# Kernel tuning notes

Hardware: AMD Instinct MI355X
Metric: run time of the kernel (lower is better)

## Reference

```python
import jax, jax.numpy as jnp
import numpy as np

N0, N1, N2 = 65536, 8192, 1024   # node counts per depth (pool factor 8, as in original m1*2=8)
DEG = 6                          # avg degree of k-space neighbor graphs
K = 10                           # number of Gaussian kernels in GMMConv


def _pool_graph(n_fine):
    # bidirectional edges between each group of 8 nodes and its representative (last node of group)
    mem = jnp.arange(n_fine)
    rep = (mem // 8) * 8 + 7
    return jnp.concatenate([mem, rep]), jnp.concatenate([rep, mem])


def setup_inputs() -> dict:
    key = jax.random.key(0)
    ks = list(jax.random.split(key, 40))
    E1, E2, E3 = DEG * N0, DEG * N1, DEG * N2
    d = {}
    d['n_feat'] = jax.random.normal(ks[0], (N0, 2), jnp.float32)
    d['src1'] = jax.random.randint(ks[1], (E1,), 0, N0)
    d['dst1'] = jax.random.randint(ks[2], (E1,), 0, N0)
    d['pkor1'] = 0.5 * jax.random.normal(ks[3], (E1, 2), jnp.float32)
    d['src2'] = jax.random.randint(ks[4], (E2,), 0, N1)
    d['dst2'] = jax.random.randint(ks[5], (E2,), 0, N1)
    d['pkor2'] = 0.5 * jax.random.normal(ks[6], (E2, 2), jnp.float32)
    d['src3'] = jax.random.randint(ks[7], (E3,), 0, N2)
    d['dst3'] = jax.random.randint(ks[8], (E3,), 0, N2)
    d['pkor3'] = 0.5 * jax.random.normal(ks[9], (E3, 2), jnp.float32)
    d['pm1_src'], d['pm1_dst'] = _pool_graph(N0)
    d['pm2_src'], d['pm2_dst'] = _pool_graph(N1)
    d['idx1'] = jnp.arange(N1) * 8 + 7
    d['idx2'] = jnp.arange(N2) * 8 + 7

    def lin(k, fi, fo):
        return jax.random.normal(k, (fi, K * fo), jnp.float32) / np.float32(np.sqrt(fi * K))

    d['W1'] = lin(ks[10], 2, 32)
    d['mu1'] = jax.random.normal(ks[11], (K, 2), jnp.float32)
    d['is1'] = jax.random.uniform(ks[12], (K, 2), jnp.float32, 0.5, 1.5)
    d['b1'] = 0.01 * jax.random.normal(ks[13], (32,), jnp.float32)
    d['W2'] = lin(ks[14], 32, 64)
    d['mu2'] = jax.random.normal(ks[15], (K, 2), jnp.float32)
    d['is2'] = jax.random.uniform(ks[16], (K, 2), jnp.float32, 0.5, 1.5)
    d['W3'] = lin(ks[17], 64, 128)
    d['mu3'] = jax.random.normal(ks[18], (K, 2), jnp.float32)
    d['is3'] = jax.random.uniform(ks[19], (K, 2), jnp.float32, 0.5, 1.5)
    d['W4'] = lin(ks[20], 192, 64)
    d['mu4'] = jax.random.normal(ks[21], (K, 2), jnp.float32)
    d['is4'] = jax.random.uniform(ks[22], (K, 2), jnp.float32, 0.5, 1.5)
    d['W5'] = lin(ks[23], 96, 40)
    d['mu5'] = jax.random.normal(ks[24], (K, 2), jnp.float32)
    d['is5'] = jax.random.uniform(ks[25], (K, 2), jnp.float32, 0.5, 1.5)
    d['b5'] = 0.01 * jax.random.normal(ks[26], (40,), jnp.float32)
    return d


def gmm_conv(x, W, mu, inv_sigma, src, dst, pseudo, n, bias=None):
    # DGL GMMConv, aggregator 'mean': h=fc(x) -> (N,K,F); gaussian edge weights over 2D pseudo coords
    h = (x @ W).reshape(x.shape[0], K, -1)                                   # (N,K,F)
    diff = pseudo[:, None, :] - mu[None, :, :]                               # (E,K,2)
    gw = jnp.exp(-0.5 * jnp.sum(diff * diff * (inv_sigma[None] ** 2), -1))   # (E,K)
    msg = h[src] * gw[:, :, None]                                            # (E,K,F)
    s = jax.ops.segment_sum(msg, dst, num_segments=n)
    deg = jax.ops.segment_sum(jnp.ones(dst.shape, x.dtype), dst, num_segments=n)
    out = jnp.sum(s / jnp.maximum(deg, 1.0)[:, None, None], axis=1)          # mean over edges, sum over kernels
    return out if bias is None else out + bias


def max_reduce(h, src, dst, n):
    # DGL update_all(copy_u, max): nodes with no in-edges get 0
    m = jax.ops.segment_max(h[src], dst, num_segments=n)
    deg = jax.ops.segment_sum(jnp.ones(dst.shape, h.dtype), dst, num_segments=n)
    return jnp.where(deg[:, None] > 0, m, jnp.zeros((), h.dtype))


def reference(n_feat, src1, dst1, pkor1, src2, dst2, pkor2, src3, dst3, pkor3,
              pm1_src, pm1_dst, pm2_src, pm2_dst, idx1, idx2,
              W1, mu1, is1, b1, W2, mu2, is2, W3, mu3, is3,
              W4, mu4, is4, W5, mu5, is5, b5):
    # encoder
    out0 = jax.nn.relu(gmm_conv(n_feat, W1, mu1, is1, src1, dst1, pkor1, N0, b1))      # (N0,32) skip0
    h = max_reduce(out0, pm1_src, pm1_dst, N0)[idx1]                                    # MaxPool -> (N1,32)
    out1 = jax.nn.relu(gmm_conv(h, W2, mu2, is2, src2, dst2, pkor2, N1))                # (N1,64) skip1
    h = max_reduce(out1, pm2_src, pm2_dst, N1)[idx2]                                    # MaxPool -> (N2,64)
    out2 = jax.nn.relu(gmm_conv(h, W3, mu3, is3, src3, dst3, pkor3, N2))                # (N2,128) bottleneck
    # decoder
    hu = jnp.zeros((N1, out2.shape[1]), out2.dtype).at[idx2].set(out2)
    hu = max_reduce(hu, pm2_src, pm2_dst, N1)                                           # UpSample -> (N1,128)
    out3 = jax.nn.relu(gmm_conv(jnp.concatenate([hu, out1], 1), W4, mu4, is4,
                                src2, dst2, pkor2, N1))                                 # (N1,64)
    hu = jnp.zeros((N0, out3.shape[1]), out3.dtype).at[idx1].set(out3)
    hu = max_reduce(hu, pm1_src, pm1_dst, N0)                                           # UpSample -> (N0,64)
    return jnp.tanh(gmm_conv(jnp.concatenate([hu, out0], 1), W5, mu5, is5,
                             src1, dst1, pkor1, N0, b5))                                # (N0,40)
```

## Files before the change

kernel.cpp:

```cpp
#include <hip/hip_runtime.h>


#define N0C 65536
#define N1C 8192
#define N2C 1024
#define KK 10

typedef _Float16 half2t __attribute__((ext_vector_type(2)));
typedef _Float16 half4 __attribute__((ext_vector_type(4)));
typedef _Float16 f16x8 __attribute__((ext_vector_type(8)));
typedef float f32x4 __attribute__((ext_vector_type(4)));

static inline int cdiv(long long a, long long b) { return (int)((a + b - 1) / b); }

__device__ __forceinline__ size_t fragi(int r, int kd, int KDT) {
    return ((size_t)(r >> 4) * KDT + (kd >> 5)) * 64 + ((kd >> 3) & 3) * 16 + (r & 15);
}


__global__ __launch_bounds__(256)
void k_hist3(const int* __restrict__ d1, const int* __restrict__ d2,
             const int* __restrict__ d3, int* __restrict__ g1,
             int* __restrict__ g2, int* __restrict__ g3,
             int E1, int E2, int E3) {
    int i = blockIdx.x * 256 + threadIdx.x;
    if (i < E1) atomicAdd(&g1[d1[i]], 1);
    else if (i < E1 + E2) atomicAdd(&g2[d2[i - E1]], 1);
    else if (i < E1 + E2 + E3) atomicAdd(&g3[d3[i - E1 - E2]], 1);
}

__device__ __forceinline__ void map_graph(int b, int& lb, int& gi) {
    if (b < 256) { gi = 0; lb = b; }
    else if (b < 288) { gi = 1; lb = b - 256; }
    else { gi = 2; lb = b - 288; }
}

__global__ __launch_bounds__(256)
void k_scan1_3(const int* __restrict__ deg1, int* __restrict__ off1,
               const int* __restrict__ deg2, int* __restrict__ off2,
               const int* __restrict__ deg3, int* __restrict__ off3,
               int* __restrict__ part) {
    __shared__ int s[256];
    int lb, gi; map_graph(blockIdx.x, lb, gi);
    const int* deg = gi == 0 ? deg1 : (gi == 1 ? deg2 : deg3);
    int* off = gi == 0 ? off1 : (gi == 1 ? off2 : off3);
    int* prt = part + (gi == 0 ? 0 : (gi == 1 ? 256 : 288));
    int i = lb * 256 + threadIdx.x;
    int v = deg[i];
    s[threadIdx.x] = v;
    __syncthreads();
#pragma unroll
    for (int d = 1; d < 256; d <<= 1) {
        int t = (threadIdx.x >= d) ? s[threadIdx.x - d] : 0;
        __syncthreads();
        s[threadIdx.x] += t;
        __syncthreads();
    }
    off[i] = s[threadIdx.x] - v;
    if (threadIdx.x == 255) prt[lb] = s[255];
}

__global__ __launch_bounds__(256)
void k_scan2_3(int* __restrict__ part) {
    __shared__ int s[256];
    int nb = blockIdx.x == 0 ? 256 : (blockIdx.x == 1 ? 32 : 4);
    int* p = part + (blockIdx.x == 0 ? 0 : (blockIdx.x == 1 ? 256 : 288));
    int v = (threadIdx.x < nb) ? p[threadIdx.x] : 0;
    s[threadIdx.x] = v;
    __syncthreads();
#pragma unroll
    for (int d = 1; d < 256; d <<= 1) {
        int t = (threadIdx.x >= d) ? s[threadIdx.x - d] : 0;
        __syncthreads();
        s[threadIdx.x] += t;
        __syncthreads();
    }
    if (threadIdx.x < nb) p[threadIdx.x] = s[threadIdx.x] - v;
}

__global__ __launch_bounds__(256)
void k_scan3_3(int* __restrict__ off1, int* __restrict__ off2, int* __restrict__ off3,
               const int* __restrict__ part,
               const int* __restrict__ deg1, const int* __restrict__ deg2,
               const int* __restrict__ deg3,
               float* __restrict__ inv1, float* __restrict__ inv2,
               float* __restrict__ inv3, int E1, int E2, int E3) {
    int lb, gi; map_graph(blockIdx.x, lb, gi);
    int* off = gi == 0 ? off1 : (gi == 1 ? off2 : off3);
    const int* deg = gi == 0 ? deg1 : (gi == 1 ? deg2 : deg3);
    float* inv = gi == 0 ? inv1 : (gi == 1 ? inv2 : inv3);
    const int* prt = part + (gi == 0 ? 0 : (gi == 1 ? 256 : 288));
    int n = gi == 0 ? N0C : (gi == 1 ? N1C : N2C);
    int E = gi == 0 ? E1 : (gi == 1 ? E2 : E3);
    int i = lb * 256 + threadIdx.x;
    off[i] += prt[lb];
    inv[i] = 1.0f / fmaxf((float)deg[i], 1.0f);
    if (i == n - 1) off[n] = E;
}

__global__ __launch_bounds__(256)
void k_scatter3(const int* __restrict__ s1, const int* __restrict__ d1,
                const float* __restrict__ p1, const int* __restrict__ o1,
                int* __restrict__ c1, int* __restrict__ cs1, float2* __restrict__ cp1,
                const int* __restrict__ s2, const int* __restrict__ d2,
                const float* __restrict__ p2, const int* __restrict__ o2,
                int* __restrict__ c2, int* __restrict__ cs2, float2* __restrict__ cp2,
                const int* __restrict__ s3, const int* __restrict__ d3,
                const float* __restrict__ p3, const int* __restrict__ o3,
                int* __restrict__ c3, int* __restrict__ cs3, float2* __restrict__ cp3,
                int E1, int E2, int E3) {
    int i = blockIdx.x * 256 + threadIdx.x;
    const int* src; const int* dst; const float* pk; const int* off;
    int* cur; int* csrc; float2* cpk; int e;
    if (i < E1) { src = s1; dst = d1; pk = p1; off = o1; cur = c1; csrc = cs1; cpk = cp1; e = i; }
    else if (i < E1 + E2) { src = s2; dst = d2; pk = p2; off = o2; cur = c2; csrc = cs2; cpk = cp2; e = i - E1; }
    else if (i < E1 + E2 + E3) { src = s3; dst = d3; pk = p3; off = o3; cur = c3; csrc = cs3; cpk = cp3; e = i - E1 - E2; }
    else return;
    int d = dst[e];
    int p = off[d] + atomicAdd(&cur[d], 1);
    csrc[p] = src[e];
    cpk[p] = reinterpret_cast<const float2*>(pk)[e];
}

__global__ __launch_bounds__(256)
void k_gw(const float2* __restrict__ cp1, const float2* __restrict__ cp2,
          const float2* __restrict__ cp3,
          const float* __restrict__ mu1, const float* __restrict__ is1,
          const float* __restrict__ mu5, const float* __restrict__ is5,
          const float* __restrict__ mu2, const float* __restrict__ is2,
          const float* __restrict__ mu4, const float* __restrict__ is4,
          const float* __restrict__ mu3, const float* __restrict__ is3,
          float* __restrict__ g1, float* __restrict__ g5, float* __restrict__ g2,
          float* __restrict__ g4, float* __restrict__ g3,
          int E1, int E2, int E3) {
    int i = blockIdx.x * 256 + threadIdx.x;
    const float2* cp; const float* mu; const float* isg; float* g; int e;
    if (i < E1) { cp = cp1; mu = mu1; isg = is1; g = g1; e = i; }
    else if (i < 2 * E1) { cp = cp1; mu = mu5; isg = is5; g = g5; e = i - E1; }
    else if (i < 2 * E1 + E2) { cp = cp2; mu = mu2; isg = is2; g = g2; e = i - 2 * E1; }
    else if (i < 2 * E1 + 2 * E2) { cp = cp2; mu = mu4; isg = is4; g = g4; e = i - 2 * E1 - E2; }
    else if (i < 2 * E1 + 2 * E2 + E3) { cp = cp3; mu = mu3; isg = is3; g = g3; e = i - 2 * E1 - 2 * E2; }
    else return;
    float2 pk = cp[e];
    float o[KK];
#pragma unroll
    for (int k = 0; k < KK; ++k) {
        float dx = (pk.x - mu[2 * k]) * isg[2 * k];
        float dy = (pk.y - mu[2 * k + 1]) * isg[2 * k + 1];
        o[k] = __expf(-0.5f * (dx * dx + dy * dy));
    }
    float4* gp = reinterpret_cast<float4*>(g + (size_t)e * 12);
    gp[0] = make_float4(o[0], o[1], o[2], o[3]);
    gp[1] = make_float4(o[4], o[5], o[6], o[7]);
    gp[2] = make_float4(o[8], o[9], 0.f, 0.f);
}

#define LOAD_G(gw, j, G)                                                     \
    float G[KK];                                                             \
    {                                                                        \
        const float4* gp_ = reinterpret_cast<const float4*>((gw) + (size_t)(j) * 12); \
        float4 g0_ = gp_[0], g1_ = gp_[1]; float2 g2_ = *reinterpret_cast<const float2*>(gp_ + 2); \
        G[0] = g0_.x; G[1] = g0_.y; G[2] = g0_.z; G[3] = g0_.w;              \
        G[4] = g1_.x; G[5] = g1_.y; G[6] = g1_.z; G[7] = g1_.w;              \
        G[8] = g2_.x; G[9] = g2_.y;                                          \
    }

__global__ __launch_bounds__(256)
void k_prep_wt(const float* __restrict__ W1, const float* __restrict__ W2,
               const float* __restrict__ W3, const float* __restrict__ W4,
               const float* __restrict__ W5,
               _Float16* __restrict__ T2,
               _Float16* __restrict__ T3, _Float16* __restrict__ T4,
               _Float16* __restrict__ T5) {
    int id = blockIdx.x * 256 + threadIdx.x;
    if (id < 20480) {
        int f = id / 320, kc = id % 320;
        T2[fragi(f, kc, 10) * 8 + (kc & 7)] = (_Float16)W2[(kc % 32) * 640 + (kc / 32) * 64 + f];
        return;
    }
    id -= 20480;
    if (id < 81920) {
        int f = id / 640, kc = id % 640;
        T3[fragi(f, kc, 20) * 8 + (kc & 7)] = (_Float16)W3[(kc % 64) * 1280 + (kc / 64) * 128 + f];
        return;
    }
    id -= 81920;
    if (id < 122880) {
        int f = id / 1920, kc = id % 1920;
        T4[fragi(f, kc, 60) * 8 + (kc & 7)] = (_Float16)W4[(kc % 192) * 640 + (kc / 192) * 64 + f];
        return;
    }
    id -= 122880;
    if (id < 46080) {
        int f = id / 960, kc = id % 960;
        float v = (f < 40) ? W5[(kc % 96) * 400 + (kc / 96) * 40 + f] : 0.0f;
        T5[fragi(f, kc, 30) * 8 + (kc & 7)] = (_Float16)v;
    }
}

__global__ __launch_bounds__(256, 3)
void k_l1(const float* __restrict__ x, const int* __restrict__ off,
          const int* __restrict__ csrc, const float* __restrict__ gw,
          const float* __restrict__ inv, const float* __restrict__ W1,
          const float* __restrict__ b1, _Float16* __restrict__ out0) {
    __shared__ float Ws[640];
    __shared__ float bs[32];
    for (int i = threadIdx.x; i < 640; i += 256) Ws[i] = W1[i];
    if (threadIdx.x < 32) bs[threadIdx.x] = b1[threadIdx.x];
    __syncthreads();
    int n = blockIdx.x * 256 + threadIdx.x;
    float a0[KK], a1[KK];
#pragma unroll
    for (int k = 0; k < KK; ++k) { a0[k] = 0.f; a1[k] = 0.f; }
    int j0 = off[n], j1 = off[n + 1];
    int j = j0;
    for (; j + 1 < j1; j += 2) {
        int sa = csrc[j];
        int sb = csrc[j + 1];
        LOAD_G(gw, j, Ga)
        LOAD_G(gw, j + 1, Gb)
        float2 xa = reinterpret_cast<const float2*>(x)[sa];
        float2 xb = reinterpret_cast<const float2*>(x)[sb];
#pragma unroll
        for (int k = 0; k < KK; ++k) {
            a0[k] = fmaf(Ga[k], xa.x, a0[k]);
            a1[k] = fmaf(Ga[k], xa.y, a1[k]);
            a0[k] = fmaf(Gb[k], xb.x, a0[k]);
            a1[k] = fmaf(Gb[k], xb.y, a1[k]);
        }
    }
    if (j < j1) {
        int sa = csrc[j];
        LOAD_G(gw, j, Ga)
        float2 xa = reinterpret_cast<const float2*>(x)[sa];
#pragma unroll
        for (int k = 0; k < KK; ++k) {
            a0[k] = fmaf(Ga[k], xa.x, a0[k]);
            a1[k] = fmaf(Ga[k], xa.y, a1[k]);
        }
    }
    float iv = inv[n];
#pragma unroll
    for (int k = 0; k < KK; ++k) { a0[k] *= iv; a1[k] *= iv; }
    _Float16* orow = out0 + (size_t)n * 32;
#pragma unroll
    for (int f4 = 0; f4 < 8; ++f4) {
        float v0 = bs[f4 * 4], v1 = bs[f4 * 4 + 1], v2 = bs[f4 * 4 + 2], v3 = bs[f4 * 4 + 3];
#pragma unroll
        for (int k = 0; k < KK; ++k) {
            const float* w0 = Ws + k * 32 + f4 * 4;
            const float* w1 = w0 + 320;
            v0 += a0[k] * w0[0] + a1[k] * w1[0];
            v1 += a0[k] * w0[1] + a1[k] * w1[1];
            v2 += a0[k] * w0[2] + a1[k] * w1[2];
            v3 += a0[k] * w0[3] + a1[k] * w1[3];
        }
        half4 o;
        o[0] = (_Float16)fmaxf(v0, 0.f); o[1] = (_Float16)fmaxf(v1, 0.f);
        o[2] = (_Float16)fmaxf(v2, 0.f); o[3] = (_Float16)fmaxf(v3, 0.f);
        *reinterpret_cast<half4*>(orow + f4 * 4) = o;
    }
}

template <int TPN>
__global__ __launch_bounds__(256, 3)
void k_aggx(const _Float16* __restrict__ xp, const int* __restrict__ off,
            const int* __restrict__ csrc, const float* __restrict__ gw,
            const float* __restrict__ inv, _Float16* __restrict__ agg, int N) {
    constexpr int CIN = TPN * 4;
    constexpr int KDT = KK * CIN / 32;
    int tid = threadIdx.x;
    int nl = tid / TPN, tt = tid - nl * TPN;
    int node = blockIdx.x * (256 / TPN) + nl;
    if (node >= N) return;
    float a[KK][4];
#pragma unroll
    for (int k = 0; k < KK; ++k)
#pragma unroll
        for (int e = 0; e < 4; ++e) a[k][e] = 0.f;
    int j0 = off[node], j1 = off[node + 1];
    int j = j0;
    for (; j + 1 < j1; j += 2) {
        int sa = csrc[j];
        int sb = csrc[j + 1];
        LOAD_G(gw, j, Ga)
        LOAD_G(gw, j + 1, Gb)
        half4 ha = *reinterpret_cast<const half4*>(xp + (size_t)sa * CIN + 4 * tt);
        half4 hb = *reinterpret_cast<const half4*>(xp + (size_t)sb * CIN + 4 * tt);
        float a0 = ha[0], a1 = ha[1], a2 = ha[2], a3 = ha[3];
        float b0 = hb[0], b1 = hb[1], b2 = hb[2], b3 = hb[3];
#pragma unroll
        for (int k = 0; k < KK; ++k) {
            a[k][0] = fmaf(Ga[k], a0, a[k][0]);
            a[k][1] = fmaf(Ga[k], a1, a[k][1]);
            a[k][2] = fmaf(Ga[k], a2, a[k][2]);
            a[k][3] = fmaf(Ga[k], a3, a[k][3]);
            a[k][0] = fmaf(Gb[k], b0, a[k][0]);
            a[k][1] = fmaf(Gb[k], b1, a[k][1]);
            a[k][2] = fmaf(Gb[k], b2, a[k][2]);
            a[k][3] = fmaf(Gb[k], b3, a[k][3]);
        }
    }
    if (j < j1) {
        int sa = csrc[j];
        LOAD_G(gw, j, Ga)
        half4 ha = *reinterpret_cast<const half4*>(xp + (size_t)sa * CIN + 4 * tt);
        float a0 = ha[0], a1 = ha[1], a2 = ha[2], a3 = ha[3];
#pragma unroll
        for (int k = 0; k < KK; ++k) {
            a[k][0] = fmaf(Ga[k], a0, a[k][0]);
            a[k][1] = fmaf(Ga[k], a1, a[k][1]);
            a[k][2] = fmaf(Ga[k], a2, a[k][2]);
            a[k][3] = fmaf(Ga[k], a3, a[k][3]);
        }
    }
    float iv = inv[node];
#pragma unroll
    for (int k = 0; k < KK; ++k) {
        half4 o;
        o[0] = (_Float16)(a[k][0] * iv); o[1] = (_Float16)(a[k][1] * iv);
        o[2] = (_Float16)(a[k][2] * iv); o[3] = (_Float16)(a[k][3] * iv);
        int kd = k * CIN + 4 * tt;
        *reinterpret_cast<half4*>(agg + fragi(node, kd, KDT) * 8 + (kd & 7)) = o;
    }
}

template <int CA, int CB, int WPB, int NPW, int NT, int ACT, int FST, int OUTH>
__global__ __launch_bounds__(WPB * 64)
void k_aggf4(const _Float16* __restrict__ xA, const _Float16* __restrict__ xB,
             const int* __restrict__ off, const int* __restrict__ csrc,
             const float* __restrict__ gw, const float* __restrict__ inv,
             const _Float16* __restrict__ Wt, const float* __restrict__ bias,
             void* __restrict__ outv, int nodeBase) {
    constexpr int CIN = CA + CB;
    constexpr int PAIRS = CIN / 2;
    constexpr int P = (PAIRS + 63) / 64;
    constexpr int KDT = KK * CIN / 32;
    constexpr int STRIDE = KK * CIN + 8;
    __shared__ _Float16 lds[16 * STRIDE];
    const int lane = threadIdx.x & 63;
    const int wv = threadIdx.x >> 6;
#pragma unroll
    for (int u = 0; u < NPW; ++u) {
        const int nl = wv * NPW + u;
        const int node = __builtin_amdgcn_readfirstlane(nodeBase + blockIdx.x * 16 + nl);
        float a[KK][2 * P];
#pragma unroll
        for (int k = 0; k < KK; ++k)
#pragma unroll
            for (int p = 0; p < 2 * P; ++p) a[k][p] = 0.f;
        int j0 = __builtin_amdgcn_readfirstlane(off[node]);
        int j1 = __builtin_amdgcn_readfirstlane(off[node + 1]);
        int deg = j1 - j0;
        if (deg > 0) {
            int pl = j0 + (lane < deg ? lane : deg - 1);
            int sall = csrc[pl];
            int e = 0;
            for (; e + 1 < deg; e += 2) {
                int sa = __builtin_amdgcn_readlane(sall, e);
                int sb = __builtin_amdgcn_readlane(sall, e + 1);
                LOAD_G(gw, j0 + e, Ga)
                LOAD_G(gw, j0 + e + 1, Gb)
                float xa0[P], xa1[P], xb0[P], xb1[P];
#pragma unroll
                for (int p = 0; p < P; ++p) {
                    int c0 = 2 * (lane + 64 * p);
                    xa0[p] = 0.f; xa1[p] = 0.f; xb0[p] = 0.f; xb1[p] = 0.f;
                    if (c0 < CIN) {
                        const _Float16* qa = (c0 < CA) ? (xA + (size_t)(sa >> 3) * CA + c0)
                                                       : (xB + (size_t)sa * CB + (c0 - CA));
                        const _Float16* qb = (c0 < CA) ? (xA + (size_t)(sb >> 3) * CA + c0)
                                                       : (xB + (size_t)sb * CB + (c0 - CA));
                        half2t ha = *reinterpret_cast<const half2t*>(qa);
                        half2t hb = *reinterpret_cast<const half2t*>(qb);
                        xa0[p] = ha[0]; xa1[p] = ha[1];
                        xb0[p] = hb[0]; xb1[p] = hb[1];
                    }
                }
#pragma unroll
                for (int k = 0; k < KK; ++k)
#pragma unroll
                    for (int p = 0; p < P; ++p) {
                        a[k][2 * p] = fmaf(Ga[k], xa0[p], a[k][2 * p]);
                        a[k][2 * p + 1] = fmaf(Ga[k], xa1[p], a[k][2 * p + 1]);
                        a[k][2 * p] = fmaf(Gb[k], xb0[p], a[k][2 * p]);
                        a[k][2 * p + 1] = fmaf(Gb[k], xb1[p], a[k][2 * p + 1]);
                    }
            }
            if (e < deg) {
                int sa = __builtin_amdgcn_readlane(sall, e);
                LOAD_G(gw, j0 + e, Ga)
                float xa0[P], xa1[P];
#pragma unroll
                for (int p = 0; p < P; ++p) {
                    int c0 = 2 * (lane + 64 * p);
                    xa0[p] = 0.f; xa1[p] = 0.f;
                    if (c0 < CIN) {
                        const _Float16* qa = (c0 < CA) ? (xA + (size_t)(sa >> 3) * CA + c0)
                                                       : (xB + (size_t)sa * CB + (c0 - CA));
                        half2t ha = *reinterpret_cast<const half2t*>(qa);
                        xa0[p] = ha[0]; xa1[p] = ha[1];
                    }
                }
#pragma unroll
                for (int k = 0; k < KK; ++k)
#pragma unroll
                    for (int p = 0; p < P; ++p) {
                        a[k][2 * p] = fmaf(Ga[k], xa0[p], a[k][2 * p]);
                        a[k][2 * p + 1] = fmaf(Ga[k], xa1[p], a[k][2 * p + 1]);
                    }
            }
        }
        float iv = inv[node];
#pragma unroll
        for (int k = 0; k < KK; ++k)
#pragma unroll
            for (int p = 0; p < P; ++p) {
                int c0 = 2 * (lane + 64 * p);
                if (c0 < CIN) {
                    half2t o;
                    o[0] = (_Float16)(a[k][2 * p] * iv);
                    o[1] = (_Float16)(a[k][2 * p + 1] * iv);
                    *reinterpret_cast<half2t*>(&lds[nl * STRIDE + k * CIN + c0]) = o;
                }
            }
    }
    __syncthreads();
    if (wv < NT) {
        const int lm = lane & 15;
        const int q = lane >> 4;
        f32x4 acc = (f32x4){0.f, 0.f, 0.f, 0.f};
        const f16x8* bp = (const f16x8*)Wt + (size_t)wv * KDT * 64 + lane;
        f16x8 af = *reinterpret_cast<const f16x8*>(&lds[lm * STRIDE + q * 8]);
        f16x8 bf = bp[0];
#pragma unroll
        for (int i = 0; i < KDT; ++i) {
            f16x8 afn, bfn;
            if (i + 1 < KDT) {
                afn = *reinterpret_cast<const f16x8*>(&lds[lm * STRIDE + (i + 1) * 32 + q * 8]);
                bfn = bp[(size_t)(i + 1) * 64];
            }
            acc = __builtin_amdgcn_mfma_f32_16x16x32_f16(af, bf, acc, 0, 0, 0);
            af = afn; bf = bfn;
        }
        int f = wv * 16 + lm;
        if (f < FST) {
            float b = bias ? bias[f] : 0.0f;
#pragma unroll
            for (int r = 0; r < 4; ++r) {
                size_t node = (size_t)nodeBase + (size_t)blockIdx.x * 16 + q * 4 + r;
                float v = acc[r] + b;
                v = (ACT == 1) ? tanhf(v) : fmaxf(v, 0.0f);
                if (OUTH) ((_Float16*)outv)[node * FST + f] = (_Float16)v;
                else ((float*)outv)[node * FST + f] = v;
            }
        }
    }
}

template <int WB, int NT, int ITERS, int ACT, int FST, int OUTH>
__global__ __launch_bounds__(WB * 64)
void k_gemm2(const _Float16* __restrict__ A, const _Float16* __restrict__ B,
             const float* __restrict__ bias, void* __restrict__ outv, int M) {
    constexpr int KDT = ITERS;
    const int lane = threadIdx.x & 63;
    const int wv = threadIdx.x >> 6;
    const int lm = lane & 15;
    const int q = lane >> 4;
    const size_t m0 = (size_t)blockIdx.y * (WB * 16) + wv * 16;
    const size_t mblk = m0 >> 4;
    f32x4 acc[NT];
#pragma unroll
    for (int t = 0; t < NT; ++t) acc[t] = (f32x4){0.f, 0.f, 0.f, 0.f};
    const f16x8* ap = (const f16x8*)A + mblk * KDT * 64 + lane;
    const f16x8* bp = (const f16x8*)B + lane;
    f16x8 af = ap[0];
    f16x8 bf[NT];
#pragma unroll
    for (int t = 0; t < NT; ++t) bf[t] = bp[(size_t)t * KDT * 64];
#pragma unroll
    for (int i = 0; i < ITERS; ++i) {
        f16x8 afn; f16x8 bfn[NT];
        if (i + 1 < ITERS) {
            afn = ap[(size_t)(i + 1) * 64];
#pragma unroll
            for (int t = 0; t < NT; ++t)
                bfn[t] = bp[((size_t)t * KDT + i + 1) * 64];
        }
#pragma unroll
        for (int t = 0; t < NT; ++t)
            acc[t] = __builtin_amdgcn_mfma_f32_16x16x32_f16(af, bf[t], acc[t], 0, 0, 0);
        af = afn;
#pragma unroll
        for (int t = 0; t < NT; ++t) bf[t] = bfn[t];
    }
#pragma unroll
    for (int t = 0; t < NT; ++t) {
        int f = t * 16 + lm;
        if (f < FST) {
            float b = bias ? bias[f] : 0.0f;
#pragma unroll
            for (int r = 0; r < 4; ++r) {
                float v = acc[t][r] + b;
                v = (ACT == 1) ? tanhf(v) : fmaxf(v, 0.0f);
                if (OUTH) ((_Float16*)outv)[(m0 + q * 4 + r) * (size_t)FST + f] = (_Float16)v;
                else ((float*)outv)[(m0 + q * 4 + r) * (size_t)FST + f] = v;
            }
        }
    }
}

__global__ __launch_bounds__(256)
void k_pool8h(const _Float16* __restrict__ in, _Float16* __restrict__ out, int total, int F) {
    int i = blockIdx.x * 256 + threadIdx.x;
    if (i >= total) return;
    int j = i / F;
    int f = i - j * F;
    const _Float16* p = in + (size_t)(j << 3) * F + f;
    float m = (float)p[0];
#pragma unroll
    for (int r = 1; r < 8; ++r) m = fmaxf(m, (float)p[(size_t)r * F]);
    out[i] = (_Float16)m;
}

extern "C" void kernel_launch(void* const* d_in, const int* in_sizes, int n_in,
                              void* d_out, int out_size, void* d_ws, size_t ws_size,
                              hipStream_t stream) {
    const float* n_feat = (const float*)d_in[0];
    const int* src1 = (const int*)d_in[1];
    const int* dst1 = (const int*)d_in[2];
    const float* pkor1 = (const float*)d_in[3];
    const int* src2 = (const int*)d_in[4];
    const int* dst2 = (const int*)d_in[5];
    const float* pkor2 = (const float*)d_in[6];
    const int* src3 = (const int*)d_in[7];
    const int* dst3 = (const int*)d_in[8];
    const float* pkor3 = (const float*)d_in[9];
    const float* W1 = (const float*)d_in[16];
    const float* mu1 = (const float*)d_in[17];
    const float* is1 = (const float*)d_in[18];
    const float* b1 = (const float*)d_in[19];
    const float* W2 = (const float*)d_in[20];
    const float* mu2 = (const float*)d_in[21];
    const float* is2 = (const float*)d_in[22];
    const float* W3 = (const float*)d_in[23];
    const float* mu3 = (const float*)d_in[24];
    const float* is3 = (const float*)d_in[25];
    const float* W4 = (const float*)d_in[26];
    const float* mu4 = (const float*)d_in[27];
    const float* is4 = (const float*)d_in[28];
    const float* W5 = (const float*)d_in[29];
    const float* mu5 = (const float*)d_in[30];
    const float* is5 = (const float*)d_in[31];
    const float* b5 = (const float*)d_in[32];

    const int E1 = in_sizes[1], E2 = in_sizes[4], E3 = in_sizes[7];
    const int NT_ = N0C + N1C + N2C;

    char* w = (char*)d_ws;
    auto alloc = [&](size_t bytes) {
        void* p = (void*)w;
        w += (bytes + 255) & ~(size_t)255;
        return p;
    };
    int* degs = (int*)alloc((size_t)NT_ * 2 * 4);
    int* deg1 = degs, *deg2 = degs + N0C, *deg3 = degs + N0C + N1C;
    int* cur1 = degs + NT_, *cur2 = cur1 + N0C, *cur3 = cur2 + N1C;
    int* off1 = (int*)alloc(((size_t)N0C + 1) * 4);
    int* off2 = (int*)alloc(((size_t)N1C + 1) * 4);
    int* off3 = (int*)alloc(((size_t)N2C + 1) * 4);
    int* part = (int*)alloc(292 * 4);
    int* csrc1 = (int*)alloc((size_t)E1 * 4);
    float2* cpk1 = (float2*)alloc((size_t)E1 * 8);
    int* csrc2 = (int*)alloc((size_t)E2 * 4);
    float2* cpk2 = (float2*)alloc((size_t)E2 * 8);
    int* csrc3 = (int*)alloc((size_t)E3 * 4);
    float2* cpk3 = (float2*)alloc((size_t)E3 * 8);
    float* inv1 = (float*)alloc((size_t)N0C * 4);
    float* inv2 = (float*)alloc((size_t)N1C * 4);
    float* inv3 = (float*)alloc((size_t)N2C * 4);
    float* g1 = (float*)alloc(((size_t)2 * E1 + 2 * E2 + E3) * 12 * 4);
    float* g5 = g1 + (size_t)E1 * 12;
    float* g2 = g5 + (size_t)E1 * 12;
    float* g4 = g2 + (size_t)E2 * 12;
    float* g3 = g4 + (size_t)E2 * 12;
    _Float16* out0 = (_Float16*)alloc((size_t)N0C * 32 * 2);
    _Float16* out1 = (_Float16*)alloc((size_t)N1C * 64 * 2);
    _Float16* out2 = (_Float16*)alloc((size_t)N2C * 128 * 2);
    _Float16* out3 = (_Float16*)alloc((size_t)N1C * 64 * 2);
    _Float16* hp1 = (_Float16*)alloc((size_t)N1C * 32 * 2);
    _Float16* hp2 = (_Float16*)alloc((size_t)N2C * 64 * 2);
    _Float16* agg2 = (_Float16*)alloc((size_t)N1C * 320 * 2);
    _Float16* agg3 = (_Float16*)alloc((size_t)N2C * 640 * 2);
    _Float16* Wt2 = (_Float16*)alloc((size_t)64 * 320 * 2);
    _Float16* Wt3 = (_Float16*)alloc((size_t)128 * 640 * 2);
    _Float16* Wt4 = (_Float16*)alloc((size_t)64 * 1920 * 2);
    _Float16* Wt5 = (_Float16*)alloc((size_t)48 * 960 * 2);

    const int ET = E1 + E2 + E3;
    const int GT = 2 * E1 + 2 * E2 + E3;

    hipMemsetAsync(degs, 0, (size_t)NT_ * 2 * 4, stream);
    k_prep_wt<<<cdiv(271360, 256), 256, 0, stream>>>(W1, W2, W3, W4, W5,
                                                     Wt2, Wt3, Wt4, Wt5);
    k_hist3<<<cdiv(ET, 256), 256, 0, stream>>>(dst1, dst2, dst3, deg1, deg2, deg3, E1, E2, E3);
    k_scan1_3<<<292, 256, 0, stream>>>(deg1, off1, deg2, off2, deg3, off3, part);
    k_scan2_3<<<3, 256, 0, stream>>>(part);
    k_scan3_3<<<292, 256, 0, stream>>>(off1, off2, off3, part, deg1, deg2, deg3,
                                       inv1, inv2, inv3, E1, E2, E3);
    k_scatter3<<<cdiv(ET, 256), 256, 0, stream>>>(
        src1, dst1, pkor1, off1, cur1, csrc1, cpk1,
        src2, dst2, pkor2, off2, cur2, csrc2, cpk2,
        src3, dst3, pkor3, off3, cur3, csrc3, cpk3, E1, E2, E3);
    k_gw<<<cdiv(GT, 256), 256, 0, stream>>>(
        cpk1, cpk2, cpk3, mu1, is1, mu5, is5, mu2, is2, mu4, is4, mu3, is3,
        g1, g5, g2, g4, g3, E1, E2, E3);

    k_l1<<<N0C / 256, 256, 0, stream>>>(n_feat, off1, csrc1, g1, inv1, W1, b1, out0);

    k_pool8h<<<cdiv(N1C * 32, 256), 256, 0, stream>>>(out0, hp1, N1C * 32, 32);
    k_aggx<8><<<cdiv(N1C, 32), 256, 0, stream>>>(hp1, off2, csrc2, g2, inv2, agg2, N1C);
    k_gemm2<2, 4, 10, 0, 64, 1><<<dim3(1, N1C / 32), 128, 0, stream>>>(agg2, Wt2, nullptr, out1, N1C);

    k_pool8h<<<cdiv(N2C * 64, 256), 256, 0, stream>>>(out1, hp2, N2C * 64, 64);
    k_aggx<16><<<cdiv(N2C, 16), 256, 0, stream>>>(hp2, off3, csrc3, g3, inv3, agg3, N2C);
    k_gemm2<1, 8, 20, 0, 128, 1><<<dim3(1, N2C / 16), 64, 0, stream>>>(agg3, Wt3, nullptr, out2, N2C);

    k_aggf4<128, 64, 16, 1, 4, 0, 64, 1><<<N1C / 16, 1024, 0, stream>>>(
        out2, out1, off2, csrc2, g4, inv2, Wt4, nullptr, out3, 0);

    k_aggf4<64, 32, 8, 2, 3, 1, 40, 0><<<N0C / 16, 512, 0, stream>>>(
        out3, out0, off1, csrc1, g5, inv1, Wt5, b5, d_out, 0);
}
```

Measured before the change: 306.5 us.

## Fuse pooling into producers, merge scans, prefetch edge metadata and weights

Replaces the three-kernel prefix scan with one kernel in which each block sums all preceding degrees itself. The degree memset moves into the weight-prep kernel, and both max-pool kernels are dropped by computing the 8-row max inside k_l1 (via shuffles) and inside the level-2 GEMM epilogue. k_aggf4 now preloads edge offsets and source indices for all of a wave's nodes up front and keeps a deeper register ring of B fragments for the MFMA loop; the last layer also changes from 8 to 4 waves per block with 4 nodes per wave. These cut launch count and intermediate memory traffic, at the cost of redundant degree summation in the scan and more register pressure.

```diff
diff --git a/kernel.cpp b/kernel.cpp
--- a/kernel.cpp
+++ b/kernel.cpp
@@ -36,15 +36,28 @@
 }
 
 __global__ __launch_bounds__(256)
-void k_scan1_3(const int* __restrict__ deg1, int* __restrict__ off1,
-               const int* __restrict__ deg2, int* __restrict__ off2,
-               const int* __restrict__ deg3, int* __restrict__ off3,
-               int* __restrict__ part) {
+void k_scanall(const int* __restrict__ deg1, int* __restrict__ off1, float* __restrict__ inv1,
+               const int* __restrict__ deg2, int* __restrict__ off2, float* __restrict__ inv2,
+               const int* __restrict__ deg3, int* __restrict__ off3, float* __restrict__ inv3,
+               int E1, int E2, int E3) {
     __shared__ int s[256];
     int lb, gi; map_graph(blockIdx.x, lb, gi);
     const int* deg = gi == 0 ? deg1 : (gi == 1 ? deg2 : deg3);
     int* off = gi == 0 ? off1 : (gi == 1 ? off2 : off3);
-    int* prt = part + (gi == 0 ? 0 : (gi == 1 ? 256 : 288));
+    float* inv = gi == 0 ? inv1 : (gi == 1 ? inv2 : inv3);
+    int n = gi == 0 ? N0C : (gi == 1 ? N1C : N2C);
+    int E = gi == 0 ? E1 : (gi == 1 ? E2 : E3);
+    int pre = 0;
+    for (int i = threadIdx.x; i < lb * 256; i += 256) pre += deg[i];
+    s[threadIdx.x] = pre;
+    __syncthreads();
+#pragma unroll
+    for (int d = 128; d > 0; d >>= 1) {
+        if (threadIdx.x < d) s[threadIdx.x] += s[threadIdx.x + d];
+        __syncthreads();
+    }
+    int base = s[0];
+    __syncthreads();
     int i = lb * 256 + threadIdx.x;
     int v = deg[i];
     s[threadIdx.x] = v;
@@ -56,45 +69,8 @@
         s[threadIdx.x] += t;
         __syncthreads();
     }
-    off[i] = s[threadIdx.x] - v;
-    if (threadIdx.x == 255) prt[lb] = s[255];
-}
-
-__global__ __launch_bounds__(256)
-void k_scan2_3(int* __restrict__ part) {
-    __shared__ int s[256];
-    int nb = blockIdx.x == 0 ? 256 : (blockIdx.x == 1 ? 32 : 4);
-    int* p = part + (blockIdx.x == 0 ? 0 : (blockIdx.x == 1 ? 256 : 288));
-    int v = (threadIdx.x < nb) ? p[threadIdx.x] : 0;
-    s[threadIdx.x] = v;
-    __syncthreads();
-#pragma unroll
-    for (int d = 1; d < 256; d <<= 1) {
-        int t = (threadIdx.x >= d) ? s[threadIdx.x - d] : 0;
-        __syncthreads();
-        s[threadIdx.x] += t;
-        __syncthreads();
-    }
-    if (threadIdx.x < nb) p[threadIdx.x] = s[threadIdx.x] - v;
-}
-
-__global__ __launch_bounds__(256)
-void k_scan3_3(int* __restrict__ off1, int* __restrict__ off2, int* __restrict__ off3,
-               const int* __restrict__ part,
-               const int* __restrict__ deg1, const int* __restrict__ deg2,
-               const int* __restrict__ deg3,
-               float* __restrict__ inv1, float* __restrict__ inv2,
-               float* __restrict__ inv3, int E1, int E2, int E3) {
-    int lb, gi; map_graph(blockIdx.x, lb, gi);
-    int* off = gi == 0 ? off1 : (gi == 1 ? off2 : off3);
-    const int* deg = gi == 0 ? deg1 : (gi == 1 ? deg2 : deg3);
-    float* inv = gi == 0 ? inv1 : (gi == 1 ? inv2 : inv3);
-    const int* prt = part + (gi == 0 ? 0 : (gi == 1 ? 256 : 288));
-    int n = gi == 0 ? N0C : (gi == 1 ? N1C : N2C);
-    int E = gi == 0 ? E1 : (gi == 1 ? E2 : E3);
-    int i = lb * 256 + threadIdx.x;
-    off[i] += prt[lb];
-    inv[i] = 1.0f / fmaxf((float)deg[i], 1.0f);
+    off[i] = base + s[threadIdx.x] - v;
+    inv[i] = 1.0f / fmaxf((float)v, 1.0f);
     if (i == n - 1) off[n] = E;
 }
 
@@ -165,14 +141,25 @@
         G[8] = g2_.x; G[9] = g2_.y;                                          \
     }
 
+#define LOAD_G2(gwp, j, G)                                                   \
+    {                                                                        \
+        const float4* gp_ = reinterpret_cast<const float4*>((gwp) + (size_t)(j) * 12); \
+        float4 g0_ = gp_[0], g1_ = gp_[1];                                   \
+        float2 g2_ = *reinterpret_cast<const float2*>(gp_ + 2);              \
+        G[0] = g0_.x; G[1] = g0_.y; G[2] = g0_.z; G[3] = g0_.w;              \
+        G[4] = g1_.x; G[5] = g1_.y; G[6] = g1_.z; G[7] = g1_.w;              \
+        G[8] = g2_.x; G[9] = g2_.y;                                          \
+    }
+
 __global__ __launch_bounds__(256)
 void k_prep_wt(const float* __restrict__ W1, const float* __restrict__ W2,
                const float* __restrict__ W3, const float* __restrict__ W4,
                const float* __restrict__ W5,
                _Float16* __restrict__ T2,
                _Float16* __restrict__ T3, _Float16* __restrict__ T4,
-               _Float16* __restrict__ T5) {
+               _Float16* __restrict__ T5, int* __restrict__ degs, int degn) {
     int id = blockIdx.x * 256 + threadIdx.x;
+    if (id < degn) degs[id] = 0;
     if (id < 20480) {
         int f = id / 320, kc = id % 320;
         T2[fragi(f, kc, 10) * 8 + (kc & 7)] = (_Float16)W2[(kc % 32) * 640 + (kc / 32) * 64 + f];
@@ -202,7 +189,8 @@
 void k_l1(const float* __restrict__ x, const int* __restrict__ off,
           const int* __restrict__ csrc, const float* __restrict__ gw,
           const float* __restrict__ inv, const float* __restrict__ W1,
-          const float* __restrict__ b1, _Float16* __restrict__ out0) {
+          const float* __restrict__ b1, _Float16* __restrict__ out0,
+          _Float16* __restrict__ hp1) {
     __shared__ float Ws[640];
     __shared__ float bs[32];
     for (int i = threadIdx.x; i < 640; i += 256) Ws[i] = W1[i];
@@ -243,6 +231,7 @@
 #pragma unroll
     for (int k = 0; k < KK; ++k) { a0[k] *= iv; a1[k] *= iv; }
     _Float16* orow = out0 + (size_t)n * 32;
+    _Float16* prow = hp1 + (size_t)(n >> 3) * 32;
 #pragma unroll
     for (int f4 = 0; f4 < 8; ++f4) {
         float v0 = bs[f4 * 4], v1 = bs[f4 * 4 + 1], v2 = bs[f4 * 4 + 2], v3 = bs[f4 * 4 + 3];
@@ -255,10 +244,25 @@
             v2 += a0[k] * w0[2] + a1[k] * w1[2];
             v3 += a0[k] * w0[3] + a1[k] * w1[3];
         }
+        v0 = fmaxf(v0, 0.f); v1 = fmaxf(v1, 0.f);
+        v2 = fmaxf(v2, 0.f); v3 = fmaxf(v3, 0.f);
         half4 o;
-        o[0] = (_Float16)fmaxf(v0, 0.f); o[1] = (_Float16)fmaxf(v1, 0.f);
-        o[2] = (_Float16)fmaxf(v2, 0.f); o[3] = (_Float16)fmaxf(v3, 0.f);
+        o[0] = (_Float16)v0; o[1] = (_Float16)v1;
+        o[2] = (_Float16)v2; o[3] = (_Float16)v3;
         *reinterpret_cast<half4*>(orow + f4 * 4) = o;
+#pragma unroll
+        for (int d = 1; d < 8; d <<= 1) {
+            v0 = fmaxf(v0, __shfl_xor(v0, d));
+            v1 = fmaxf(v1, __shfl_xor(v1, d));
+            v2 = fmaxf(v2, __shfl_xor(v2, d));
+            v3 = fmaxf(v3, __shfl_xor(v3, d));
+        }
+        if ((threadIdx.x & 7) == 0) {
+            half4 p;
+            p[0] = (_Float16)v0; p[1] = (_Float16)v1;
+            p[2] = (_Float16)v2; p[3] = (_Float16)v3;
+            *reinterpret_cast<half4*>(prow + f4 * 4) = p;
+        }
     }
 }
 
@@ -340,76 +344,87 @@
     __shared__ _Float16 lds[16 * STRIDE];
     const int lane = threadIdx.x & 63;
     const int wv = threadIdx.x >> 6;
+    int j0u[NPW], degu[NPW], sallu[NPW];
+#pragma unroll
+    for (int u = 0; u < NPW; ++u) {
+        const int node = __builtin_amdgcn_readfirstlane(nodeBase + blockIdx.x * 16 + wv * NPW + u);
+        j0u[u] = __builtin_amdgcn_readfirstlane(off[node]);
+        int j1 = __builtin_amdgcn_readfirstlane(off[node + 1]);
+        degu[u] = j1 - j0u[u];
+        int pl = (degu[u] > 0) ? (j0u[u] + (lane < degu[u] ? lane : degu[u] - 1)) : 0;
+        sallu[u] = csrc[pl];
+    }
 #pragma unroll
     for (int u = 0; u < NPW; ++u) {
         const int nl = wv * NPW + u;
         const int node = __builtin_amdgcn_readfirstlane(nodeBase + blockIdx.x * 16 + nl);
+        const int j0 = j0u[u];
+        const int deg = degu[u];
+        const int sall = sallu[u];
         float a[KK][2 * P];
 #pragma unroll
         for (int k = 0; k < KK; ++k)
 #pragma unroll
             for (int p = 0; p < 2 * P; ++p) a[k][p] = 0.f;
-        int j0 = __builtin_amdgcn_readfirstlane(off[node]);
-        int j1 = __builtin_amdgcn_readfirstlane(off[node + 1]);
-        int deg = j1 - j0;
-        if (deg > 0) {
-            int pl = j0 + (lane < deg ? lane : deg - 1);
-            int sall = csrc[pl];
-            int e = 0;
-            for (; e + 1 < deg; e += 2) {
-                int sa = __builtin_amdgcn_readlane(sall, e);
-                int sb = __builtin_amdgcn_readlane(sall, e + 1);
-                LOAD_G(gw, j0 + e, Ga)
-                LOAD_G(gw, j0 + e + 1, Gb)
-                float xa0[P], xa1[P], xb0[P], xb1[P];
+        int e = 0;
+        for (; e + 1 < deg; e += 2) {
+            int sa = __builtin_amdgcn_readlane(sall, e);
+            int sb = __builtin_amdgcn_readlane(sall, e + 1);
+            int gj = __builtin_amdgcn_readfirstlane(j0 + e);
+            float Ga[KK], Gb[KK];
+            LOAD_G2(gw, gj, Ga)
+            LOAD_G2(gw, gj + 1, Gb)
+            float xa0[P], xa1[P], xb0[P], xb1[P];
+#pragma unroll
+            for (int p = 0; p < P; ++p) {
+                int c0 = 2 * (lane + 64 * p);
+                xa0[p] = 0.f; xa1[p] = 0.f; xb0[p] = 0.f; xb1[p] = 0.f;
+                if (c0 < CIN) {
+                    bool useA = c0 < CA;
+                    const _Float16* qa = useA ? (xA + (size_t)(sa >> 3) * CA + c0)
+                                              : (xB + (size_t)sa * CB + (c0 - CA));
+                    const _Float16* qb = useA ? (xA + (size_t)(sb >> 3) * CA + c0)
+                                              : (xB + (size_t)sb * CB + (c0 - CA));
+                    half2t ha = *reinterpret_cast<const half2t*>(qa);
+                    half2t hb = *reinterpret_cast<const half2t*>(qb);
+                    xa0[p] = ha[0]; xa1[p] = ha[1];
+                    xb0[p] = hb[0]; xb1[p] = hb[1];
+                }
+            }
+#pragma unroll
+            for (int k = 0; k < KK; ++k)
 #pragma unroll
                 for (int p = 0; p < P; ++p) {
-                    int c0 = 2 * (lane + 64 * p);
-                    xa0[p] = 0.f; xa1[p] = 0.f; xb0[p] = 0.f; xb1[p] = 0.f;
-                    if (c0 < CIN) {
-                        const _Float16* qa = (c0 < CA) ? (xA + (size_t)(sa >> 3) * CA + c0)
-                                                       : (xB + (size_t)sa * CB + (c0 - CA));
-                        const _Float16* qb = (c0 < CA) ? (xA + (size_t)(sb >> 3) * CA + c0)
-                                                       : (xB + (size_t)sb * CB + (c0 - CA));
-                        half2t ha = *reinterpret_cast<const half2t*>(qa);
-                        half2t hb = *reinterpret_cast<const half2t*>(qb);
-                        xa0[p] = ha[0]; xa1[p] = ha[1];
-                        xb0[p] = hb[0]; xb1[p] = hb[1];
-                    }
+                    a[k][2 * p] = fmaf(Ga[k], xa0[p], a[k][2 * p]);
+                    a[k][2 * p + 1] = fmaf(Ga[k], xa1[p], a[k][2 * p + 1]);
+                    a[k][2 * p] = fmaf(Gb[k], xb0[p], a[k][2 * p]);
+                    a[k][2 * p + 1] = fmaf(Gb[k], xb1[p], a[k][2 * p + 1]);
                 }
-#pragma unroll
-                for (int k = 0; k < KK; ++k)
-#pragma unroll
-                    for (int p = 0; p < P; ++p) {
-                        a[k][2 * p] = fmaf(Ga[k], xa0[p], a[k][2 * p]);
-                        a[k][2 * p + 1] = fmaf(Ga[k], xa1[p], a[k][2 * p + 1]);
-                        a[k][2 * p] = fmaf(Gb[k], xb0[p], a[k][2 * p]);
-                        a[k][2 * p + 1] = fmaf(Gb[k], xb1[p], a[k][2 * p + 1]);
-                    }
+        }
+        if (e < deg) {
+            int sa = __builtin_amdgcn_readlane(sall, e);
+            int gj = __builtin_amdgcn_readfirstlane(j0 + e);
+            float Ga[KK];
+            LOAD_G2(gw, gj, Ga)
+            float xa0[P], xa1[P];
+#pragma unroll
+            for (int p = 0; p < P; ++p) {
+                int c0 = 2 * (lane + 64 * p);
+                xa0[p] = 0.f; xa1[p] = 0.f;
+                if (c0 < CIN) {
+                    const _Float16* qa = (c0 < CA) ? (xA + (size_t)(sa >> 3) * CA + c0)
+                                                   : (xB + (size_t)sa * CB + (c0 - CA));
+                    half2t ha = *reinterpret_cast<const half2t*>(qa);
+                    xa0[p] = ha[0]; xa1[p] = ha[1];
+                }
             }
-            if (e < deg) {
-                int sa = __builtin_amdgcn_readlane(sall, e);
-                LOAD_G(gw, j0 + e, Ga)
-                float xa0[P], xa1[P];
+#pragma unroll
+            for (int k = 0; k < KK; ++k)
 #pragma unroll
                 for (int p = 0; p < P; ++p) {
-                    int c0 = 2 * (lane + 64 * p);
-                    xa0[p] = 0.f; xa1[p] = 0.f;
-                    if (c0 < CIN) {
-                        const _Float16* qa = (c0 < CA) ? (xA + (size_t)(sa >> 3) * CA + c0)
-                                                       : (xB + (size_t)sa * CB + (c0 - CA));
-                        half2t ha = *reinterpret_cast<const half2t*>(qa);
-                        xa0[p] = ha[0]; xa1[p] = ha[1];
-                    }
+                    a[k][2 * p] = fmaf(Ga[k], xa0[p], a[k][2 * p]);
+                    a[k][2 * p + 1] = fmaf(Ga[k], xa1[p], a[k][2 * p + 1]);
                 }
-#pragma unroll
-                for (int k = 0; k < KK; ++k)
-#pragma unroll
-                    for (int p = 0; p < P; ++p) {
-                        a[k][2 * p] = fmaf(Ga[k], xa0[p], a[k][2 * p]);
-                        a[k][2 * p + 1] = fmaf(Ga[k], xa1[p], a[k][2 * p + 1]);
-                    }
-            }
         }
         float iv = inv[node];
 #pragma unroll
@@ -425,23 +440,28 @@
                 }
             }
     }
+    constexpr int PF = (KDT < 8) ? KDT : 8;
+    const int lm = lane & 15;
+    const int q = lane >> 4;
+    const f16x8* bp = (const f16x8*)Wt + (size_t)wv * KDT * 64 + lane;
+    f16x8 bfr[PF];
+    if (wv < NT) {
+#pragma unroll
+        for (int i = 0; i < PF; ++i) bfr[i] = bp[(size_t)i * 64];
+    }
     __syncthreads();
     if (wv < NT) {
-        const int lm = lane & 15;
-        const int q = lane >> 4;
         f32x4 acc = (f32x4){0.f, 0.f, 0.f, 0.f};
-        const f16x8* bp = (const f16x8*)Wt + (size_t)wv * KDT * 64 + lane;
         f16x8 af = *reinterpret_cast<const f16x8*>(&lds[lm * STRIDE + q * 8]);
-        f16x8 bf = bp[0];
 #pragma unroll
         for (int i = 0; i < KDT; ++i) {
-            f16x8 afn, bfn;
-            if (i + 1 < KDT) {
+            f16x8 afn;
+            if (i + 1 < KDT)
                 afn = *reinterpret_cast<const f16x8*>(&lds[lm * STRIDE + (i + 1) * 32 + q * 8]);
-                bfn = bp[(size_t)(i + 1) * 64];
-            }
-            acc = __builtin_amdgcn_mfma_f32_16x16x32_f16(af, bf, acc, 0, 0, 0);
-            af = afn; bf = bfn;
+            f16x8 b = bfr[i % PF];
+            if (i + PF < KDT) bfr[i % PF] = bp[(size_t)(i + PF) * 64];
+            acc = __builtin_amdgcn_mfma_f32_16x16x32_f16(af, b, acc, 0, 0, 0);
+            af = afn;
         }
         int f = wv * 16 + lm;
         if (f < FST) {
@@ -458,10 +478,11 @@
     }
 }
 
-template <int WB, int NT, int ITERS, int ACT, int FST, int OUTH>
+template <int WB, int NT, int ITERS, int ACT, int FST, int OUTH, int POOL>
 __global__ __launch_bounds__(WB * 64)
 void k_gemm2(const _Float16* __restrict__ A, const _Float16* __restrict__ B,
-             const float* __restrict__ bias, void* __restrict__ outv, int M) {
+             const float* __restrict__ bias, void* __restrict__ outv,
+             _Float16* __restrict__ poolout, int M) {
     constexpr int KDT = ITERS;
     const int lane = threadIdx.x & 63;
     const int wv = threadIdx.x >> 6;
@@ -499,28 +520,25 @@
         int f = t * 16 + lm;
         if (f < FST) {
             float b = bias ? bias[f] : 0.0f;
+            float vr[4];
 #pragma unroll
             for (int r = 0; r < 4; ++r) {
                 float v = acc[t][r] + b;
-                v = (ACT == 1) ? tanhf(v) : fmaxf(v, 0.0f);
-                if (OUTH) ((_Float16*)outv)[(m0 + q * 4 + r) * (size_t)FST + f] = (_Float16)v;
-                else ((float*)outv)[(m0 + q * 4 + r) * (size_t)FST + f] = v;
+                vr[r] = (ACT == 1) ? tanhf(v) : fmaxf(v, 0.0f);
             }
-        }
-    }
-}
-
-__global__ __launch_bounds__(256)
-void k_pool8h(const _Float16* __restrict__ in, _Float16* __restrict__ out, int total, int F) {
-    int i = blockIdx.x * 256 + threadIdx.x;
-    if (i >= total) return;
-    int j = i / F;
-    int f = i - j * F;
-    const _Float16* p = in + (size_t)(j << 3) * F + f;
-    float m = (float)p[0];
-#pragma unroll
-    for (int r = 1; r < 8; ++r) m = fmaxf(m, (float)p[(size_t)r * F]);
-    out[i] = (_Float16)m;
+#pragma unroll
+            for (int r = 0; r < 4; ++r) {
+                if (OUTH) ((_Float16*)outv)[(m0 + q * 4 + r) * (size_t)FST + f] = (_Float16)vr[r];
+                else ((float*)outv)[(m0 + q * 4 + r) * (size_t)FST + f] = vr[r];
+            }
+            if (POOL) {
+                float m = fmaxf(fmaxf(vr[0], vr[1]), fmaxf(vr[2], vr[3]));
+                m = fmaxf(m, __shfl_xor(m, 16));
+                if ((q & 1) == 0)
+                    poolout[(size_t)((m0 >> 3) + (q >> 1)) * FST + f] = (_Float16)m;
+            }
+        }
+    }
 }
 
 extern "C" void kernel_launch(void* const* d_in, const int* in_sizes, int n_in,
@@ -569,7 +587,6 @@
     int* off1 = (int*)alloc(((size_t)N0C + 1) * 4);
     int* off2 = (int*)alloc(((size_t)N1C + 1) * 4);
     int* off3 = (int*)alloc(((size_t)N2C + 1) * 4);
-    int* part = (int*)alloc(292 * 4);
     int* csrc1 = (int*)alloc((size_t)E1 * 4);
     float2* cpk1 = (float2*)alloc((size_t)E1 * 8);
     int* csrc2 = (int*)alloc((size_t)E2 * 4);
@@ -600,14 +617,12 @@
     const int ET = E1 + E2 + E3;
     const int GT = 2 * E1 + 2 * E2 + E3;
 
-    hipMemsetAsync(degs, 0, (size_t)NT_ * 2 * 4, stream);
     k_prep_wt<<<cdiv(271360, 256), 256, 0, stream>>>(W1, W2, W3, W4, W5,
-                                                     Wt2, Wt3, Wt4, Wt5);
+                                                     Wt2, Wt3, Wt4, Wt5,
+                                                     degs, NT_ * 2);
     k_hist3<<<cdiv(ET, 256), 256, 0, stream>>>(dst1, dst2, dst3, deg1, deg2, deg3, E1, E2, E3);
-    k_scan1_3<<<292, 256, 0, stream>>>(deg1, off1, deg2, off2, deg3, off3, part);
-    k_scan2_3<<<3, 256, 0, stream>>>(part);
-    k_scan3_3<<<292, 256, 0, stream>>>(off1, off2, off3, part, deg1, deg2, deg3,
-                                       inv1, inv2, inv3, E1, E2, E3);
+    k_scanall<<<292, 256, 0, stream>>>(deg1, off1, inv1, deg2, off2, inv2,
+                                       deg3, off3, inv3, E1, E2, E3);
     k_scatter3<<<cdiv(ET, 256), 256, 0, stream>>>(
         src1, dst1, pkor1, off1, cur1, csrc1, cpk1,
         src2, dst2, pkor2, off2, cur2, csrc2, cpk2,
@@ -616,19 +631,17 @@
         cpk1, cpk2, cpk3, mu1, is1, mu5, is5, mu2, is2, mu4, is4, mu3, is3,
         g1, g5, g2, g4, g3, E1, E2, E3);
 
-    k_l1<<<N0C / 256, 256, 0, stream>>>(n_feat, off1, csrc1, g1, inv1, W1, b1, out0);
-
-    k_pool8h<<<cdiv(N1C * 32, 256), 256, 0, stream>>>(out0, hp1, N1C * 32, 32);
+    k_l1<<<N0C / 256, 256, 0, stream>>>(n_feat, off1, csrc1, g1, inv1, W1, b1, out0, hp1);
+
     k_aggx<8><<<cdiv(N1C, 32), 256, 0, stream>>>(hp1, off2, csrc2, g2, inv2, agg2, N1C);
-    k_gemm2<2, 4, 10, 0, 64, 1><<<dim3(1, N1C / 32), 128, 0, stream>>>(agg2, Wt2, nullptr, out1, N1C);
-
-    k_pool8h<<<cdiv(N2C * 64, 256), 256, 0, stream>>>(out1, hp2, N2C * 64, 64);
+    k_gemm2<2, 4, 10, 0, 64, 1, 1><<<dim3(1, N1C / 32), 128, 0, stream>>>(agg2, Wt2, nullptr, out1, hp2, N1C);
+
     k_aggx<16><<<cdiv(N2C, 16), 256, 0, stream>>>(hp2, off3, csrc3, g3, inv3, agg3, N2C);
-    k_gemm2<1, 8, 20, 0, 128, 1><<<dim3(1, N2C / 16), 64, 0, stream>>>(agg3, Wt3, nullptr, out2, N2C);
+    k_gemm2<1, 8, 20, 0, 128, 1, 0><<<dim3(1, N2C / 16), 64, 0, stream>>>(agg3, Wt3, nullptr, out2, nullptr, N2C);
 
     k_aggf4<128, 64, 16, 1, 4, 0, 64, 1><<<N1C / 16, 1024, 0, stream>>>(
         out2, out1, off2, csrc2, g4, inv2, Wt4, nullptr, out3, 0);
 
-    k_aggf4<64, 32, 8, 2, 3, 1, 40, 0><<<N0C / 16, 512, 0, stream>>>(
+    k_aggf4<64, 32, 4, 4, 3, 1, 40, 0><<<N0C / 16, 256, 0, stream>>>(
         out3, out0, off1, csrc1, g5, inv1, Wt5, b5, d_out, 0);
 }
```

New measurement: 346.5 us. +13.1%, slower.
